# Performance work log

Hardware: AMD Instinct MI355X
Metric: run time of the kernel (lower is better)

The kernel has to match this reference:

```python
import jax, jax.numpy as jnp
import numpy as np
import math

B, S, D = 2, 2048, 1024
H, HKV = 16, 4
HD = D // H
NREP = H // HKV
E, TOPK, SHARED = 8, 2, 1
HIDDEN = 684
AUX_COEF = 0.01
RMS_EPS = 1e-5


def setup_inputs() -> dict:
    key = jax.random.key(0)
    ks = jax.random.split(key, 14)
    def w(k, shape):
        return jax.random.normal(k, shape, jnp.float32) * 0.02
    # standard RoPE angles, base 10000
    t = jnp.arange(S, dtype=jnp.float32)
    inv = 1.0 / (10000.0 ** (jnp.arange(0, HD, 2, dtype=jnp.float32) / HD))
    ang = t[:, None] * inv[None, :]  # [S, HD//2]
    return {
        "x": jax.random.normal(ks[0], (B, S, D), jnp.float32),
        "freqs_cos": jnp.cos(ang),
        "freqs_sin": jnp.sin(ang),
        "wq": w(ks[1], (D, D)),
        "wk": w(ks[2], (D, HKV * HD)),
        "wv": w(ks[3], (D, HKV * HD)),
        "wo": w(ks[4], (D, D)),
        "router_w": w(ks[5], (D, E)),
        "ew1": w(ks[6], (E, D, HIDDEN)),
        "ew2": w(ks[7], (E, HIDDEN, D)),
        "ew3": w(ks[8], (E, D, HIDDEN)),
        "sw1": w(ks[9], (SHARED, D, HIDDEN)),
        "sw2": w(ks[10], (SHARED, HIDDEN, D)),
        "sw3": w(ks[11], (SHARED, D, HIDDEN)),
        "g_attn": jnp.ones((D,), jnp.float32),
        "g_ffn": jnp.ones((D,), jnp.float32),
        "start_pos": 0,
    }


def rmsnorm(x, g, eps=RMS_EPS):
    xf = x.astype(jnp.float32)
    n = xf * jax.lax.rsqrt(jnp.mean(xf * xf, axis=-1, keepdims=True) + eps)
    return g * n.astype(x.dtype)


def rope(x, cos, sin):
    # pairs are consecutive elements (view_as_complex of reshape(..., -1, 2))
    xr, xi = x[..., 0::2], x[..., 1::2]
    c = cos[None, :, None, :]  # [1,S,1,HD//2]
    s = sin[None, :, None, :]
    r = xr * c - xi * s
    i = xr * s + xi * c
    return jnp.stack([r, i], axis=-1).reshape(x.shape)


def attention(x, freqs_cos, freqs_sin, wq, wk, wv, wo):
    b, s, d = x.shape
    q = (x @ wq).reshape(b, s, H, HD)
    k = (x @ wk).reshape(b, s, HKV, HD)
    v = (x @ wv).reshape(b, s, HKV, HD)
    q = rope(q, freqs_cos, freqs_sin)
    k = rope(k, freqs_cos, freqs_sin)
    k = jnp.repeat(k, NREP, axis=2)
    v = jnp.repeat(v, NREP, axis=2)
    q, k, v = (t.transpose(0, 2, 1, 3) for t in (q, k, v))  # [B,H,S,HD]
    att = jnp.einsum('bhqd,bhkd->bhqk', q, k) * (1.0 / math.sqrt(HD))
    # faithful to torch: tril then masked_fill(att == 0, -inf)
    tri = jnp.tril(jnp.ones((s, s), bool))
    att = jnp.where(tri, att, 0.0)
    att = jnp.where(att == 0.0, -jnp.inf, att)
    att = jax.nn.softmax(att, axis=-1)
    out = jnp.einsum('bhqk,bhkd->bhqd', att, v)
    out = out.transpose(0, 2, 1, 3).reshape(b, s, d)
    return out @ wo


def moe(x, router_w, ew1, ew2, ew3, sw1, sw2, sw3):
    b, s, d = x.shape
    xf = x.reshape(-1, d)                       # [N, D]
    logits = xf @ router_w                      # [N, E]
    probs = jax.nn.softmax(logits, axis=-1)
    _, topk_idx = jax.lax.top_k(logits, TOPK)   # [N, K]
    topk_p, _ = jax.lax.top_k(probs, TOPK)      # same ordering (softmax monotone)
    density = jnp.mean(jax.nn.one_hot(topk_idx[:, 0], E, dtype=jnp.float32), axis=0)
    aux = AUX_COEF * jnp.sum(density * jnp.mean(probs, axis=0)) * E
    # per-token combine weight over experts [N, E]
    onehot = jax.nn.one_hot(topk_idx, E, dtype=xf.dtype)  # [N, K, E]
    cw = jnp.einsum('nk,nke->ne', topk_p, onehot)
    # dense expert evaluation (jit-friendly dispatch/combine equivalent)
    h = jax.nn.silu(jnp.einsum('nd,edh->neh', xf, ew1)) * jnp.einsum('nd,edh->neh', xf, ew3)
    eo = jnp.einsum('neh,ehd->ned', h, ew2)
    out = jnp.einsum('ne,ned->nd', cw, eo)
    for i in range(SHARED):
        out = out + (jax.nn.silu(xf @ sw1[i]) * (xf @ sw3[i])) @ sw2[i]
    return out.reshape(b, s, d), aux


def reference(x, freqs_cos, freqs_sin, wq, wk, wv, wo, router_w, ew1, ew2, ew3, sw1, sw2, sw3, g_attn, g_ffn, start_pos):
    h = x + attention(rmsnorm(x, g_attn), freqs_cos, freqs_sin, wq, wk, wv, wo)
    ffn_out, aux = moe(rmsnorm(h, g_ffn), router_w, ew1, ew2, ew3, sw1, sw2, sw3)
    return h + ffn_out, aux
```

## Files before the change

### kernel.cpp

```cpp
#include <hip/hip_runtime.h>
#include <hip/hip_bf16.h>
#include <cstdint>

#define B_ 2
#define S_ 2048
#define D_ 1024
#define H_ 16
#define HKV_ 4
#define HD_ 64
#define E_ 8
#define HIDDEN_ 684
#define NT_ (B_*S_)
#define NEGBIG (-1e30f)

using bf16 = __hip_bfloat16;
typedef __attribute__((ext_vector_type(8))) short short8v;
typedef __attribute__((ext_vector_type(4))) short short4v;
typedef __attribute__((ext_vector_type(4))) float f32x4;

static __device__ __forceinline__ float b2f(bf16 v){ return __bfloat162float(v); }
static __device__ __forceinline__ bf16 f2b(float v){ return __float2bfloat16(v); }
static __device__ __forceinline__ short f2bs(float v){ bf16 h = f2b(v); return *reinterpret_cast<short*>(&h); }
static __device__ __forceinline__ float dload(const void* p, size_t i, int isbf){
  return isbf ? b2f(((const bf16*)p)[i]) : ((const float*)p)[i];
}

__global__ void k_detect(const uint32_t* __restrict__ g, int* __restrict__ flag, int* __restrict__ cnt){
  if(threadIdx.x == 0 && blockIdx.x == 0){
    uint32_t w0 = g[0], w1 = g[1], w2 = g[2], w3 = g[3];
    int bf;
    if(w0==0x3F803F80u && w1==0x3F803F80u && w2==0x3F803F80u && w3==0x3F803F80u) bf = 1;
    else if(w0==0x3F800000u && w1==0x3F800000u && w2==0x3F800000u && w3==0x3F800000u) bf = 0;
    else bf = 1;
    flag[0] = bf;
  }
  if(threadIdx.x < E_ && blockIdx.x == 0) cnt[threadIdx.x] = 0;
}

__global__ __launch_bounds__(256) void k_rms(const void* __restrict__ X, const void* __restrict__ g,
                                             bf16* __restrict__ outb, float* __restrict__ outf,
                                             const int* __restrict__ flag, int xdyn){
  int isbf = flag[0]; int xb = xdyn ? isbf : 0;
  int t = blockIdx.x; int tid = threadIdx.x;
  float v[4]; float ss = 0.f;
  #pragma unroll
  for(int i=0;i<4;i++){ v[i] = dload(X, (size_t)t*D_ + tid + i*256, xb); ss += v[i]*v[i]; }
  __shared__ float red[256];
  red[tid] = ss; __syncthreads();
  for(int st=128; st>0; st>>=1){ if(tid<st) red[tid] += red[tid+st]; __syncthreads(); }
  float r = rsqrtf(red[0]*(1.f/(float)D_) + 1e-5f);
  #pragma unroll
  for(int i=0;i<4;i++){
    int d = tid + i*256;
    float val = v[i]*r*dload(g, d, isbf);
    outb[(size_t)t*D_ + d] = f2b(val);
    if(outf) outf[(size_t)t*D_ + d] = val;
  }
}

#define ASTRIDE 40

static __device__ __forceinline__ f32x4 mfma16(short8v a, short8v b, f32x4 c){
  return __builtin_amdgcn_mfma_f32_16x16x32_bf16(a, b, c, 0, 0, 0);
}

template<int AMAP, int OMODE>
__global__ __launch_bounds__(256) void k_mgemm(
    const bf16* __restrict__ A, const void* __restrict__ Bw, void* __restrict__ Cout,
    const void* __restrict__ resid,
    int M, int N, int K, int ldc,
    const int* __restrict__ cnt, const int* __restrict__ offs, const int* __restrict__ list,
    const int* __restrict__ flag)
{
  int isbf = flag[0];
  int e, ct, rt;
  int base = 0; size_t eoff = 0;
  if(cnt){
    e = blockIdx.x;
    int nc = (N+63)>>6;
    ct = blockIdx.y % nc; rt = blockIdx.y / nc;
    M = cnt[e]; if(M<0) M=0; if(M>NT_) M=NT_;
    base = offs[e];
    eoff = (size_t)e*(size_t)K*(size_t)N;
  } else {
    e = 0; ct = blockIdx.x; rt = blockIdx.y;
  }
  int m0 = rt*128; if(m0 >= M) return;
  int n0 = ct*64;

  __shared__ short As[2][128*ASTRIDE];
  __shared__ short Bs[2][64*ASTRIDE];
  __shared__ int rowA[128];

  int tid = threadIdx.x;
  int w = tid>>6, l = tid&63, lr = l&15, lg = l>>4;

  if(tid < 128){
    int rloc = m0 + tid;
    int ar = -1;
    if(rloc < M) ar = (AMAP==2) ? (list[e*NT_ + rloc]>>1) : (base + rloc);
    rowA[tid] = ar;
  }
  __syncthreads();

  int srow = tid>>1, skh = (tid&1)*16;
  int keya = (srow>>4)&3, kb0 = skh>>3;
  int bk = tid>>3, bnc = (tid&7)*8;
  int keyb = ((tid&7)>>1)&3;
  int bcol = (((bk>>3)^keyb)<<3) + (bk&7);
  int arow = rowA[srow];

  short8v rA0, rA1, rB;

  auto loadAB = [&](int kt){
    int k0 = kt*32;
    {
      short tmp[16];
      if(arow >= 0 && k0+skh+16 <= K){
        const short4v* src = (const short4v*)(A + (size_t)arow*K + k0 + skh);
        #pragma unroll
        for(int c=0;c<4;c++) *(short4v*)&tmp[c*4] = src[c];
      } else {
        #pragma unroll
        for(int i=0;i<16;i++){
          int gk = k0+skh+i;
          short v = 0;
          if(arow>=0 && gk<K) v = *(const short*)&A[(size_t)arow*K+gk];
          tmp[i] = v;
        }
      }
      #pragma unroll
      for(int i=0;i<8;i++){ rA0[i]=tmp[i]; rA1[i]=tmp[8+i]; }
    }
    {
      int gk = k0 + bk;
      short tmp[8];
      if(gk < K && n0+bnc+8 <= N){
        size_t bb = eoff + (size_t)gk*N + n0 + bnc;
        if(isbf){
          const short4v* src = (const short4v*)((const bf16*)Bw + bb);
          *(short4v*)&tmp[0] = src[0];
          *(short4v*)&tmp[4] = src[1];
        } else {
          const f32x4* src = (const f32x4*)((const float*)Bw + bb);
          f32x4 f0 = src[0], f1 = src[1];
          #pragma unroll
          for(int i=0;i<4;i++){ tmp[i]=f2bs(f0[i]); tmp[4+i]=f2bs(f1[i]); }
        }
      } else {
        #pragma unroll
        for(int i=0;i<8;i++){
          int gn = n0+bnc+i;
          float v = 0.f;
          if(gk<K && gn<N) v = dload(Bw, eoff + (size_t)gk*N + gn, isbf);
          tmp[i] = f2bs(v);
        }
      }
      #pragma unroll
      for(int i=0;i<8;i++) rB[i]=tmp[i];
    }
  };
  auto writeAB = [&](int buf){
    *(short8v*)&As[buf][srow*ASTRIDE + ((kb0^keya)<<3)]     = rA0;
    *(short8v*)&As[buf][srow*ASTRIDE + (((kb0+1)^keya)<<3)] = rA1;
    #pragma unroll
    for(int i=0;i<8;i++) Bs[buf][(bnc+i)*ASTRIDE + bcol] = rB[i];
  };

  f32x4 acc[2][4] = {};
  int KT = (K+31)>>5;

  loadAB(0); writeAB(0);
  __syncthreads();
  int cur = 0;
  for(int kt=0; kt<KT; ++kt){
    bool more = (kt+1 < KT);
    if(more) loadAB(kt+1);
    short8v a[2], b[4];
    #pragma unroll
    for(int fi=0;fi<2;fi++)
      a[fi] = *(const short8v*)&As[cur][(w*32+fi*16+lr)*ASTRIDE + ((lg^((w*2+fi)&3))<<3)];
    #pragma unroll
    for(int fj=0;fj<4;fj++)
      b[fj] = *(const short8v*)&Bs[cur][(fj*16+lr)*ASTRIDE + ((lg^fj)<<3)];
    #pragma unroll
    for(int fi=0;fi<2;fi++)
      #pragma unroll
      for(int fj=0;fj<4;fj++)
        acc[fi][fj] = mfma16(a[fi], b[fj], acc[fi][fj]);
    if(more){ writeAB(cur^1); cur ^= 1; }
    __syncthreads();
  }

  #pragma unroll
  for(int fi=0;fi<2;fi++){
    #pragma unroll
    for(int r=0;r<4;r++){
      int rl = m0 + w*32 + fi*16 + lg*4 + r;
      if(rl >= M) continue;
      int orow;
      if(OMODE==2){ orow = list[e*NT_ + rl]; if(orow<0||orow>=2*NT_) continue; }
      else orow = base + rl;
      #pragma unroll
      for(int fj=0;fj<4;fj++){
        int gcol = n0 + fj*16 + lr;
        if(gcol >= N) continue;
        float v = acc[fi][fj][r];
        size_t o = (size_t)orow*ldc + gcol;
        if(OMODE==1)      ((float*)Cout)[o] = v + dload(resid, o, isbf);
        else if(OMODE==2) ((bf16*)Cout)[o] = f2b(v);
        else if(OMODE==3) ((float*)Cout)[o] = ((float*)Cout)[o] + v;
        else              ((bf16*)Cout)[o] = f2b(v);
      }
    }
  }
}

__global__ __launch_bounds__(256) void k_qkv(
    const bf16* __restrict__ A, const void* __restrict__ Wq, const void* __restrict__ Wk,
    const void* __restrict__ Wv, bf16* __restrict__ Oq, bf16* __restrict__ Ok, bf16* __restrict__ Ov,
    const int* __restrict__ flag)
{
  int isbf = flag[0];
  int ct = blockIdx.x, rt = blockIdx.y;
  const void* Bw; bf16* Cout; int N, n0;
  if(ct < 16){ Bw = Wq; Cout = Oq; N = D_;  n0 = ct*64; }
  else if(ct < 20){ Bw = Wk; Cout = Ok; N = 256; n0 = (ct-16)*64; }
  else { Bw = Wv; Cout = Ov; N = 256; n0 = (ct-20)*64; }
  const int K = D_, M = NT_;
  int m0 = rt*128;

  __shared__ short As[2][128*ASTRIDE];
  __shared__ short Bs[2][64*ASTRIDE];

  int tid = threadIdx.x;
  int w = tid>>6, l = tid&63, lr = l&15, lg = l>>4;

  int srow = tid>>1, skh = (tid&1)*16;
  int keya = (srow>>4)&3, kb0 = skh>>3;
  int bk = tid>>3, bnc = (tid&7)*8;
  int keyb = ((tid&7)>>1)&3;
  int bcol = (((bk>>3)^keyb)<<3) + (bk&7);
  int arow = m0 + srow;

  short8v rA0, rA1, rB;

  auto loadAB = [&](int kt){
    int k0 = kt*32;
    {
      short tmp[16];
      const short4v* src = (const short4v*)(A + (size_t)arow*K + k0 + skh);
      #pragma unroll
      for(int c=0;c<4;c++) *(short4v*)&tmp[c*4] = src[c];
      #pragma unroll
      for(int i=0;i<8;i++){ rA0[i]=tmp[i]; rA1[i]=tmp[8+i]; }
    }
    {
      int gk = k0 + bk;
      short tmp[8];
      size_t bb = (size_t)gk*N + n0 + bnc;
      if(isbf){
        const short4v* src = (const short4v*)((const bf16*)Bw + bb);
        *(short4v*)&tmp[0] = src[0];
        *(short4v*)&tmp[4] = src[1];
      } else {
        const f32x4* src = (const f32x4*)((const float*)Bw + bb);
        f32x4 f0 = src[0], f1 = src[1];
        #pragma unroll
        for(int i=0;i<4;i++){ tmp[i]=f2bs(f0[i]); tmp[4+i]=f2bs(f1[i]); }
      }
      #pragma unroll
      for(int i=0;i<8;i++) rB[i]=tmp[i];
    }
  };
  auto writeAB = [&](int buf){
    *(short8v*)&As[buf][srow*ASTRIDE + ((kb0^keya)<<3)]     = rA0;
    *(short8v*)&As[buf][srow*ASTRIDE + (((kb0+1)^keya)<<3)] = rA1;
    #pragma unroll
    for(int i=0;i<8;i++) Bs[buf][(bnc+i)*ASTRIDE + bcol] = rB[i];
  };

  f32x4 acc[2][4] = {};
  int KT = K>>5;

  loadAB(0); writeAB(0);
  __syncthreads();
  int cur = 0;
  for(int kt=0; kt<KT; ++kt){
    bool more = (kt+1 < KT);
    if(more) loadAB(kt+1);
    short8v a[2], b[4];
    #pragma unroll
    for(int fi=0;fi<2;fi++)
      a[fi] = *(const short8v*)&As[cur][(w*32+fi*16+lr)*ASTRIDE + ((lg^((w*2+fi)&3))<<3)];
    #pragma unroll
    for(int fj=0;fj<4;fj++)
      b[fj] = *(const short8v*)&Bs[cur][(fj*16+lr)*ASTRIDE + ((lg^fj)<<3)];
    #pragma unroll
    for(int fi=0;fi<2;fi++)
      #pragma unroll
      for(int fj=0;fj<4;fj++)
        acc[fi][fj] = mfma16(a[fi], b[fj], acc[fi][fj]);
    if(more){ writeAB(cur^1); cur ^= 1; }
    __syncthreads();
  }

  #pragma unroll
  for(int fi=0;fi<2;fi++){
    #pragma unroll
    for(int r=0;r<4;r++){
      int rl = m0 + w*32 + fi*16 + lg*4 + r;
      if(rl >= M) continue;
      #pragma unroll
      for(int fj=0;fj<4;fj++){
        int gcol = n0 + fj*16 + lr;
        Cout[(size_t)rl*N + gcol] = f2b(acc[fi][fj][r]);
      }
    }
  }
}

__global__ __launch_bounds__(256) void k_ffn1m(
    const bf16* __restrict__ A, const void* __restrict__ W1e, const void* __restrict__ W3e,
    const void* __restrict__ W1s, const void* __restrict__ W3s,
    bf16* __restrict__ OutE, bf16* __restrict__ OutS,
    const int* __restrict__ cnt, const int* __restrict__ offs, const int* __restrict__ list,
    const int* __restrict__ flag)
{
  int isbf = flag[0];
  const int K = D_, N = HIDDEN_;
  int e = blockIdx.x, y = blockIdx.y;
  int ct, rt, M, base, gat;
  const void* W1; const void* W3; bf16* Out;
  size_t eoff;
  if(y < 352){
    ct = y / 32; rt = y % 32;
    M = cnt[e]; if(M<0) M=0; if(M>NT_) M=NT_;
    base = offs[e]; gat = 1;
    W1 = W1e; W3 = W3e; Out = OutE;
    eoff = (size_t)e*(size_t)K*(size_t)N;
  } else {
    int ys = (y-352)*8 + e;
    ct = ys / 32; rt = ys % 32;
    M = NT_; base = 0; gat = 0;
    W1 = W1s; W3 = W3s; Out = OutS;
    eoff = 0;
  }
  int m0 = rt*128; if(m0 >= M) return;
  int n0 = ct*64;

  __shared__ short As[2][128*ASTRIDE];
  __shared__ short B1s[2][64*ASTRIDE];
  __shared__ short B3s[2][64*ASTRIDE];
  __shared__ int rowA[128];

  int tid = threadIdx.x;
  int w = tid>>6, l = tid&63, lr = l&15, lg = l>>4;

  if(tid < 128){
    int rloc = m0 + tid;
    int ar = -1;
    if(rloc < M) ar = gat ? (list[e*NT_ + rloc]>>1) : rloc;
    rowA[tid] = ar;
  }
  __syncthreads();

  int srow = tid>>1, skh = (tid&1)*16;
  int keya = (srow>>4)&3, kb0 = skh>>3;
  int bk = tid>>3, bnc = (tid&7)*8;
  int keyb = ((tid&7)>>1)&3;
  int bcol = (((bk>>3)^keyb)<<3) + (bk&7);
  int arow = rowA[srow];

  short8v rA0, rA1, rB1, rB3;

  auto loadB = [&](const void* Bw, int kt, short8v& rB){
    int k0 = kt*32;
    int gk = k0 + bk;
    short tmp[8];
    if(gk < K && n0+bnc+8 <= N){
      size_t bb = eoff + (size_t)gk*N + n0 + bnc;
      if(isbf){
        const short4v* src = (const short4v*)((const bf16*)Bw + bb);
        *(short4v*)&tmp[0] = src[0];
        *(short4v*)&tmp[4] = src[1];
      } else {
        const f32x4* src = (const f32x4*)((const float*)Bw + bb);
        f32x4 f0 = src[0], f1 = src[1];
        #pragma unroll
        for(int i=0;i<4;i++){ tmp[i]=f2bs(f0[i]); tmp[4+i]=f2bs(f1[i]); }
      }
    } else {
      #pragma unroll
      for(int i=0;i<8;i++){
        int gn = n0+bnc+i;
        float v = 0.f;
        if(gk<K && gn<N) v = dload(Bw, eoff + (size_t)gk*N + gn, isbf);
        tmp[i] = f2bs(v);
      }
    }
    #pragma unroll
    for(int i=0;i<8;i++) rB[i]=tmp[i];
  };
  auto loadA = [&](int kt){
    int k0 = kt*32;
    short tmp[16];
    if(arow >= 0 && k0+skh+16 <= K){
      const short4v* src = (const short4v*)(A + (size_t)arow*K + k0 + skh);
      #pragma unroll
      for(int c=0;c<4;c++) *(short4v*)&tmp[c*4] = src[c];
    } else {
      #pragma unroll
      for(int i=0;i<16;i++){
        int gk = k0+skh+i;
        short v = 0;
        if(arow>=0 && gk<K) v = *(const short*)&A[(size_t)arow*K+gk];
        tmp[i] = v;
      }
    }
    #pragma unroll
    for(int i=0;i<8;i++){ rA0[i]=tmp[i]; rA1[i]=tmp[8+i]; }
  };
  auto writeAll = [&](int buf){
    *(short8v*)&As[buf][srow*ASTRIDE + ((kb0^keya)<<3)]     = rA0;
    *(short8v*)&As[buf][srow*ASTRIDE + (((kb0+1)^keya)<<3)] = rA1;
    #pragma unroll
    for(int i=0;i<8;i++){
      B1s[buf][(bnc+i)*ASTRIDE + bcol] = rB1[i];
      B3s[buf][(bnc+i)*ASTRIDE + bcol] = rB3[i];
    }
  };

  f32x4 a1[2][4] = {}, a3[2][4] = {};
  int KT = (K+31)>>5;

  loadA(0); loadB(W1, 0, rB1); loadB(W3, 0, rB3); writeAll(0);
  __syncthreads();
  int cur = 0;
  for(int kt=0; kt<KT; ++kt){
    bool more = (kt+1 < KT);
    if(more){ loadA(kt+1); loadB(W1, kt+1, rB1); loadB(W3, kt+1, rB3); }
    short8v a[2], b1[4], b3[4];
    #pragma unroll
    for(int fi=0;fi<2;fi++)
      a[fi] = *(const short8v*)&As[cur][(w*32+fi*16+lr)*ASTRIDE + ((lg^((w*2+fi)&3))<<3)];
    #pragma unroll
    for(int fj=0;fj<4;fj++){
      b1[fj] = *(const short8v*)&B1s[cur][(fj*16+lr)*ASTRIDE + ((lg^fj)<<3)];
      b3[fj] = *(const short8v*)&B3s[cur][(fj*16+lr)*ASTRIDE + ((lg^fj)<<3)];
    }
    #pragma unroll
    for(int fi=0;fi<2;fi++)
      #pragma unroll
      for(int fj=0;fj<4;fj++){
        a1[fi][fj] = mfma16(a[fi], b1[fj], a1[fi][fj]);
        a3[fi][fj] = mfma16(a[fi], b3[fj], a3[fi][fj]);
      }
    if(more){ writeAll(cur^1); cur ^= 1; }
    __syncthreads();
  }

  #pragma unroll
  for(int fi=0;fi<2;fi++){
    #pragma unroll
    for(int r=0;r<4;r++){
      int rl = m0 + w*32 + fi*16 + lg*4 + r;
      if(rl >= M) continue;
      int orow = base + rl;
      #pragma unroll
      for(int fj=0;fj<4;fj++){
        int gcol = n0 + fj*16 + lr;
        if(gcol >= N) continue;
        float sg = a1[fi][fj][r];
        float v = (sg/(1.f+__expf(-sg))) * a3[fi][fj][r];
        Out[(size_t)orow*N + gcol] = f2b(v);
      }
    }
  }
}

__global__ __launch_bounds__(256) void k_ffn2m(
    const bf16* __restrict__ Ae, const bf16* __restrict__ Ash,
    const void* __restrict__ W2e, const void* __restrict__ W2s,
    bf16* __restrict__ OutE, float* __restrict__ OutS,
    const int* __restrict__ cnt, const int* __restrict__ offs, const int* __restrict__ list,
    const int* __restrict__ flag)
{
  int isbf = flag[0];
  const int K = HIDDEN_, N = D_;
  int e = blockIdx.x, y = blockIdx.y;
  int ct, rt, M, base, exm;
  const bf16* A; const void* Bw;
  size_t eoff;
  if(y < 512){
    ct = y / 32; rt = y % 32;
    M = cnt[e]; if(M<0) M=0; if(M>NT_) M=NT_;
    base = offs[e]; exm = 1;
    A = Ae; Bw = W2e;
    eoff = (size_t)e*(size_t)K*(size_t)N;
  } else {
    int ys = (y-512)*8 + e;
    ct = ys / 32; rt = ys % 32;
    M = NT_; base = 0; exm = 0;
    A = Ash; Bw = W2s;
    eoff = 0;
  }
  int m0 = rt*128; if(m0 >= M) return;
  int n0 = ct*64;

  __shared__ short As[2][128*ASTRIDE];
  __shared__ short Bs[2][64*ASTRIDE];

  int tid = threadIdx.x;
  int w = tid>>6, l = tid&63, lr = l&15, lg = l>>4;

  int srow = tid>>1, skh = (tid&1)*16;
  int keya = (srow>>4)&3, kb0 = skh>>3;
  int bk = tid>>3, bnc = (tid&7)*8;
  int keyb = ((tid&7)>>1)&3;
  int bcol = (((bk>>3)^keyb)<<3) + (bk&7);
  int arow = (m0 + srow < M) ? (base + m0 + srow) : -1;

  short8v rA0, rA1, rB;

  auto loadAB = [&](int kt){
    int k0 = kt*32;
    {
      short tmp[16];
      if(arow >= 0 && k0+skh+16 <= K){
        const short4v* src = (const short4v*)(A + (size_t)arow*K + k0 + skh);
        #pragma unroll
        for(int c=0;c<4;c++) *(short4v*)&tmp[c*4] = src[c];
      } else {
        #pragma unroll
        for(int i=0;i<16;i++){
          int gk = k0+skh+i;
          short v = 0;
          if(arow>=0 && gk<K) v = *(const short*)&A[(size_t)arow*K+gk];
          tmp[i] = v;
        }
      }
      #pragma unroll
      for(int i=0;i<8;i++){ rA0[i]=tmp[i]; rA1[i]=tmp[8+i]; }
    }
    {
      int gk = k0 + bk;
      short tmp[8];
      if(gk < K && n0+bnc+8 <= N){
        size_t bb = eoff + (size_t)gk*N + n0 + bnc;
        if(isbf){
          const short4v* src = (const short4v*)((const bf16*)Bw + bb);
          *(short4v*)&tmp[0] = src[0];
          *(short4v*)&tmp[4] = src[1];
        } else {
          const f32x4* src = (const f32x4*)((const float*)Bw + bb);
          f32x4 f0 = src[0], f1 = src[1];
          #pragma unroll
          for(int i=0;i<4;i++){ tmp[i]=f2bs(f0[i]); tmp[4+i]=f2bs(f1[i]); }
        }
      } else {
        #pragma unroll
        for(int i=0;i<8;i++){
          int gn = n0+bnc+i;
          float v = 0.f;
          if(gk<K && gn<N) v = dload(Bw, eoff + (size_t)gk*N + gn, isbf);
          tmp[i] = f2bs(v);
        }
      }
      #pragma unroll
      for(int i=0;i<8;i++) rB[i]=tmp[i];
    }
  };
  auto writeAB = [&](int buf){
    *(short8v*)&As[buf][srow*ASTRIDE + ((kb0^keya)<<3)]     = rA0;
    *(short8v*)&As[buf][srow*ASTRIDE + (((kb0+1)^keya)<<3)] = rA1;
    #pragma unroll
    for(int i=0;i<8;i++) Bs[buf][(bnc+i)*ASTRIDE + bcol] = rB[i];
  };

  f32x4 acc[2][4] = {};
  int KT = (K+31)>>5;

  loadAB(0); writeAB(0);
  __syncthreads();
  int cur = 0;
  for(int kt=0; kt<KT; ++kt){
    bool more = (kt+1 < KT);
    if(more) loadAB(kt+1);
    short8v a[2], b[4];
    #pragma unroll
    for(int fi=0;fi<2;fi++)
      a[fi] = *(const short8v*)&As[cur][(w*32+fi*16+lr)*ASTRIDE + ((lg^((w*2+fi)&3))<<3)];
    #pragma unroll
    for(int fj=0;fj<4;fj++)
      b[fj] = *(const short8v*)&Bs[cur][(fj*16+lr)*ASTRIDE + ((lg^fj)<<3)];
    #pragma unroll
    for(int fi=0;fi<2;fi++)
      #pragma unroll
      for(int fj=0;fj<4;fj++)
        acc[fi][fj] = mfma16(a[fi], b[fj], acc[fi][fj]);
    if(more){ writeAB(cur^1); cur ^= 1; }
    __syncthreads();
  }

  #pragma unroll
  for(int fi=0;fi<2;fi++){
    #pragma unroll
    for(int r=0;r<4;r++){
      int rl = m0 + w*32 + fi*16 + lg*4 + r;
      if(rl >= M) continue;
      if(exm){
        int orow = list[e*NT_ + rl];
        if(orow<0||orow>=2*NT_) continue;
        #pragma unroll
        for(int fj=0;fj<4;fj++){
          int gcol = n0 + fj*16 + lr;
          OutE[(size_t)orow*N + gcol] = f2b(acc[fi][fj][r]);
        }
      } else {
        #pragma unroll
        for(int fj=0;fj<4;fj++){
          int gcol = n0 + fj*16 + lr;
          size_t o = (size_t)rl*N + gcol;
          OutS[o] = OutS[o] + acc[fi][fj][r];
        }
      }
    }
  }
}

__global__ __launch_bounds__(256) void k_rope(bf16* __restrict__ ql, bf16* __restrict__ kl,
                                              const void* __restrict__ fc, const void* __restrict__ fs,
                                              const int* __restrict__ flag){
  int isbf = flag[0];
  int t = blockIdx.x; int s = t % S_;
  int tid = threadIdx.x;
  for(int p0 = tid; p0 < 512; p0 += 256){
    int h = p0>>5, p = p0&31;
    float c = dload(fc, s*32+p, isbf), sn = dload(fs, s*32+p, isbf);
    size_t o = (size_t)t*D_ + h*64 + 2*p;
    float xr = b2f(ql[o]), xi = b2f(ql[o+1]);
    ql[o]   = f2b(xr*c - xi*sn);
    ql[o+1] = f2b(xr*sn + xi*c);
  }
  if(tid < 128){
    int h = tid>>5, p = tid&31;
    float c = dload(fc, s*32+p, isbf), sn = dload(fs, s*32+p, isbf);
    size_t o = (size_t)t*256 + h*64 + 2*p;
    float xr = b2f(kl[o]), xi = b2f(kl[o+1]);
    kl[o]   = f2b(xr*c - xi*sn);
    kl[o+1] = f2b(xr*sn + xi*c);
  }
}

#define TST 72

__global__ __launch_bounds__(256) void k_attn(const bf16* __restrict__ Q, const bf16* __restrict__ Kg,
                                              const bf16* __restrict__ V, bf16* __restrict__ Out){
  int qt_ = (S_/64 - 1) - blockIdx.x;
  int h = blockIdx.y, b = blockIdx.z;
  int kvh = h>>2;
  const bf16* qb = Q + (size_t)b*S_*D_ + h*HD_;
  const bf16* kb = Kg + (size_t)b*S_*256 + kvh*HD_;
  const bf16* vb = V  + (size_t)b*S_*256 + kvh*HD_;
  __shared__ short Qs[64*TST];
  __shared__ short Ks[64*TST];
  __shared__ short Vt[64*TST];
  __shared__ short Ps[4][16*TST];
  int tid = threadIdx.x;
  int w = tid>>6, l = tid&63, lr = l&15, lg = l>>4;
  int sr = tid>>2, sc0 = (tid&3)*16;
  int vc = (((sr>>3)^(tid&3))<<3) + (sr&7);

  {
    const short8v* src = (const short8v*)(qb + (size_t)(qt_*64 + sr)*D_ + sc0);
    *(short8v*)&Qs[sr*TST + sc0]     = src[0];
    *(short8v*)&Qs[sr*TST + sc0 + 8] = src[1];
  }
  __syncthreads();
  short8v aQ0 = *(const short8v*)&Qs[(w*16+lr)*TST + lg*8];
  short8v aQ1 = *(const short8v*)&Qs[(w*16+lr)*TST + lg*8 + 32];

  float mreg[4], lreg[4];
  f32x4 accO[4] = {};
  #pragma unroll
  for(int r=0;r<4;r++){ mreg[r] = NEGBIG; lreg[r] = 0.f; }

  for(int kt=0; kt<=qt_; ++kt){
    __syncthreads();
    {
      const short8v* ksrc = (const short8v*)(kb + (size_t)(kt*64 + sr)*256 + sc0);
      *(short8v*)&Ks[sr*TST + sc0]     = ksrc[0];
      *(short8v*)&Ks[sr*TST + sc0 + 8] = ksrc[1];
      const short8v* vsrc = (const short8v*)(vb + (size_t)(kt*64 + sr)*256 + sc0);
      short8v v0 = vsrc[0], v1 = vsrc[1];
      #pragma unroll
      for(int i=0;i<8;i++){
        Vt[(sc0+i)*TST + vc]   = v0[i];
        Vt[(sc0+8+i)*TST + vc] = v1[i];
      }
    }
    __syncthreads();
    f32x4 s[4];
    #pragma unroll
    for(int fj=0; fj<4; fj++){
      short8v b0 = *(const short8v*)&Ks[(fj*16+lr)*TST + lg*8];
      short8v b1 = *(const short8v*)&Ks[(fj*16+lr)*TST + lg*8 + 32];
      f32x4 z = {};
      z = mfma16(aQ0, b0, z);
      z = mfma16(aQ1, b1, z);
      s[fj] = z;
    }
    #pragma unroll
    for(int fj=0; fj<4; fj++)
      #pragma unroll
      for(int r=0;r<4;r++){
        float v = s[fj][r]*0.125f;
        if(kt==qt_ && (fj*16+lr) > (w*16+lg*4+r)) v = NEGBIG;
        s[fj][r] = v;
      }
    float p[4][4], sc[4];
    #pragma unroll
    for(int r=0;r<4;r++){
      float mx = fmaxf(fmaxf(s[0][r],s[1][r]), fmaxf(s[2][r],s[3][r]));
      mx = fmaxf(mx, __shfl_xor(mx,1,64));
      mx = fmaxf(mx, __shfl_xor(mx,2,64));
      mx = fmaxf(mx, __shfl_xor(mx,4,64));
      mx = fmaxf(mx, __shfl_xor(mx,8,64));
      float mn = fmaxf(mreg[r], mx);
      sc[r] = __expf(mreg[r]-mn);
      float ps = 0.f;
      #pragma unroll
      for(int fj=0;fj<4;fj++){ float pv = __expf(s[fj][r]-mn); p[fj][r] = pv; ps += pv; }
      ps += __shfl_xor(ps,1,64); ps += __shfl_xor(ps,2,64);
      ps += __shfl_xor(ps,4,64); ps += __shfl_xor(ps,8,64);
      lreg[r] = lreg[r]*sc[r] + ps;
      mreg[r] = mn;
    }
    #pragma unroll
    for(int fj=0;fj<4;fj++)
      #pragma unroll
      for(int r=0;r<4;r++)
        accO[fj][r] *= sc[r];
    #pragma unroll
    for(int fj=0;fj<4;fj++)
      #pragma unroll
      for(int r=0;r<4;r++)
        Ps[w][(lg*4+r)*TST + fj*16+lr] = f2bs(p[fj][r]);
    short8v a0 = *(const short8v*)&Ps[w][lr*TST + lg*8];
    short8v a1 = *(const short8v*)&Ps[w][lr*TST + lg*8 + 32];
    #pragma unroll
    for(int fj=0;fj<4;fj++){
      int row = fj*16+lr;
      short8v b0 = *(const short8v*)&Vt[row*TST + ((lg^fj)<<3)];
      short8v b1 = *(const short8v*)&Vt[row*TST + (((lg^fj)+4)<<3)];
      accO[fj] = mfma16(a0, b0, accO[fj]);
      accO[fj] = mfma16(a1, b1, accO[fj]);
    }
  }
  #pragma unroll
  for(int r=0;r<4;r++){
    int qr = qt_*64 + w*16 + lg*4 + r;
    float inv = (lreg[r] > 0.f) ? 1.f/lreg[r] : 0.f;
    #pragma unroll
    for(int fj=0;fj<4;fj++)
      Out[((size_t)(b*S_+qr))*D_ + h*HD_ + fj*16+lr] = f2b(accO[fj][r]*inv);
  }
}

__global__ __launch_bounds__(64) void k_router(const float* __restrict__ X, const void* __restrict__ W,
                                               float* __restrict__ probs, float* __restrict__ p01,
                                               int* __restrict__ idx0buf, int* __restrict__ list,
                                               int* __restrict__ cnt, const int* __restrict__ flag){
  int isbf = flag[0];
  int t = blockIdx.x; int lane = threadIdx.x;
  float pe[8] = {};
  if(isbf){
    const bf16* Wb = (const bf16*)W;
    for(int d = lane; d < D_; d += 64){
      float xv = X[(size_t)t*D_ + d];
      #pragma unroll
      for(int e=0;e<8;e++) pe[e] += xv*b2f(Wb[(size_t)d*E_+e]);
    }
  } else {
    const float* Wf = (const float*)W;
    for(int d = lane; d < D_; d += 64){
      float xv = X[(size_t)t*D_ + d];
      #pragma unroll
      for(int e=0;e<8;e++) pe[e] += xv*Wf[(size_t)d*E_+e];
    }
  }
  for(int msk=1;msk<64;msk<<=1)
    #pragma unroll
    for(int e=0;e<8;e++) pe[e] += __shfl_xor(pe[e], msk, 64);
  if(lane == 0){
    float mx = pe[0];
    #pragma unroll
    for(int e=1;e<8;e++) mx = fmaxf(mx, pe[e]);
    float pr[8], sum = 0.f;
    #pragma unroll
    for(int e=0;e<8;e++){ pr[e] = __expf(pe[e]-mx); sum += pr[e]; }
    #pragma unroll
    for(int e=0;e<8;e++){ pr[e] /= sum; probs[t*8+e] = pr[e]; }
    int i0 = 0;
    #pragma unroll
    for(int e=1;e<8;e++) if(pe[e] > pe[i0]) i0 = e;
    int i1 = -1;
    #pragma unroll
    for(int e=0;e<8;e++){ if(e==i0) continue; if(i1<0 || pe[e] > pe[i1]) i1 = e; }
    p01[t*2]   = pr[i0];
    p01[t*2+1] = pr[i1];
    idx0buf[t] = i0;
    int pos = atomicAdd(&cnt[i0], 1);
    if(pos >= 0 && pos < NT_) list[i0*NT_ + pos] = t*2;
    pos     = atomicAdd(&cnt[i1], 1);
    if(pos >= 0 && pos < NT_) list[i1*NT_ + pos] = t*2 + 1;
  }
}

__global__ __launch_bounds__(256) void k_stats(const float* __restrict__ probs, const int* __restrict__ idx0buf,
                                               float* __restrict__ cnt0f, float* __restrict__ psum){
  int e = blockIdx.x; int tid = threadIdx.x;
  float sp = 0.f, sc = 0.f;
  for(int n = tid; n < NT_; n += 256){ sp += probs[n*8+e]; sc += (idx0buf[n]==e) ? 1.f : 0.f; }
  __shared__ float r1[256], r2[256];
  r1[tid] = sp; r2[tid] = sc; __syncthreads();
  for(int st=128; st>0; st>>=1){ if(tid<st){ r1[tid]+=r1[tid+st]; r2[tid]+=r2[tid+st]; } __syncthreads(); }
  if(tid==0){ psum[e] = r1[0]; cnt0f[e] = r2[0]; }
}

__global__ void k_finish(const float* __restrict__ cnt0f, const float* __restrict__ psum,
                         const int* __restrict__ cnt, int* __restrict__ offs,
                         bf16* __restrict__ auxb, float* __restrict__ auxf, const int* __restrict__ flag){
  if(threadIdx.x==0 && blockIdx.x==0){
    int o = 0;
    for(int e=0;e<8;e++){ offs[e] = o; int c = cnt[e]; if(c < 0) c = 0; if(c > NT_) c = NT_; o += c; }
    float aux = 0.f;
    for(int e=0;e<8;e++) aux += (cnt0f[e]*(1.f/(float)NT_))*(psum[e]*(1.f/(float)NT_));
    float v = aux*0.01f*8.f;
    if(flag[0]) auxb[0] = f2b(v); else auxf[0] = v;
  }
}

__global__ __launch_bounds__(256) void k_combine(const float* __restrict__ hbuf, const bf16* __restrict__ eosl,
                                                 const float* __restrict__ p01,
                                                 bf16* __restrict__ outb, float* __restrict__ outf,
                                                 const int* __restrict__ flag){
  int t = blockIdx.x; int tid = threadIdx.x;
  int isbf = flag[0];
  float p0 = p01[t*2], p1 = p01[t*2+1];
  #pragma unroll
  for(int i=0;i<4;i++){
    int d = tid + i*256;
    float v = hbuf[(size_t)t*D_ + d]
            + p0*b2f(eosl[((size_t)(t*2))*D_ + d])
            + p1*b2f(eosl[((size_t)(t*2+1))*D_ + d]);
    size_t o = (size_t)t*D_ + d;
    if(isbf) outb[o] = f2b(v); else outf[o] = v;
  }
}

static const size_t O_HBUF = 0;
static const size_t O_XNB  = 16777216;
static const size_t O_QLIN = 25165824;
static const size_t O_KLIN = 33554432;
static const size_t O_VLIN = 35651584;
static const size_t O_AOUT = 37748736;
static const size_t O_XN2B = 16777216;
static const size_t O_XN2F = 25165824;
static const size_t O_HEXP = 46137344;
static const size_t O_SHH  = 57344000;
static const size_t O_EOSL = 16777216;
static const size_t O_PROBS= 62947328;
static const size_t O_P01  = 63078400;
static const size_t O_IDX0 = 63111168;
static const size_t O_LIST = 63127552;
static const size_t O_CNT  = 63258624;
static const size_t O_CNT0 = 63258656;
static const size_t O_PSUM = 63258688;
static const size_t O_OFFS = 63258720;
static const size_t O_FLAG = 63258752;

extern "C" void kernel_launch(void* const* d_in, const int* in_sizes, int n_in,
                              void* d_out, int out_size, void* d_ws, size_t ws_size,
                              hipStream_t stream){
  (void)in_sizes; (void)n_in; (void)out_size; (void)ws_size;
  char* ws = (char*)d_ws;
  float* hbuf = (float*)(ws + O_HBUF);
  bf16* xnb   = (bf16*)(ws + O_XNB);
  bf16* qlin  = (bf16*)(ws + O_QLIN);
  bf16* klin  = (bf16*)(ws + O_KLIN);
  bf16* vlin  = (bf16*)(ws + O_VLIN);
  bf16* aout  = (bf16*)(ws + O_AOUT);
  bf16* xn2b  = (bf16*)(ws + O_XN2B);
  float* xn2f = (float*)(ws + O_XN2F);
  bf16* hexp  = (bf16*)(ws + O_HEXP);
  bf16* shh   = (bf16*)(ws + O_SHH);
  bf16* eosl  = (bf16*)(ws + O_EOSL);
  float* probs=(float*)(ws + O_PROBS);
  float* p01 = (float*)(ws + O_P01);
  int*  idx0 = (int*)(ws + O_IDX0);
  int*  list = (int*)(ws + O_LIST);
  int*  cnt  = (int*)(ws + O_CNT);
  float* cnt0f=(float*)(ws + O_CNT0);
  float* psum= (float*)(ws + O_PSUM);
  int*  offs = (int*)(ws + O_OFFS);
  int*  flg  = (int*)(ws + O_FLAG);

  bf16* outb = (bf16*)d_out;
  float* outf = (float*)d_out;
  bf16* auxb = outb + (size_t)NT_*D_;
  float* auxf = outf + (size_t)NT_*D_;

  k_detect<<<1, 64, 0, stream>>>((const uint32_t*)d_in[14], flg, cnt);

  k_rms<<<NT_, 256, 0, stream>>>(d_in[0], d_in[14], xnb, nullptr, flg, 1);

  k_qkv<<<dim3(24,32), 256, 0, stream>>>(xnb, d_in[3], d_in[4], d_in[5], qlin, klin, vlin, flg);

  k_rope<<<NT_, 256, 0, stream>>>(qlin, klin, d_in[1], d_in[2], flg);

  k_attn<<<dim3(S_/64, H_, B_), 256, 0, stream>>>(qlin, klin, vlin, aout);

  k_mgemm<0,1><<<dim3(16,32), 256, 0, stream>>>(aout, d_in[6], hbuf, d_in[0], NT_, D_, D_, D_, nullptr, nullptr, nullptr, flg);

  k_rms<<<NT_, 256, 0, stream>>>(hbuf, d_in[15], xn2b, xn2f, flg, 0);

  k_router<<<NT_, 64, 0, stream>>>(xn2f, d_in[7], probs, p01, idx0, list, cnt, flg);
  k_stats<<<E_, 256, 0, stream>>>(probs, idx0, cnt0f, psum);
  k_finish<<<1, 64, 0, stream>>>(cnt0f, psum, cnt, offs, auxb, auxf, flg);

  k_ffn1m<<<dim3(E_, 352+44), 256, 0, stream>>>(xn2b, d_in[8], d_in[10], d_in[11], d_in[13],
                                                hexp, shh, cnt, offs, list, flg);

  k_ffn2m<<<dim3(E_, 512+64), 256, 0, stream>>>(hexp, shh, d_in[9], d_in[12],
                                                eosl, hbuf, cnt, offs, list, flg);

  k_combine<<<NT_, 256, 0, stream>>>(hbuf, eosl, p01, outb, outf, flg);
}
```

Measured before the change: 625.0 us.

## Unroll FFN GEMM K-loops by two with dual register prefetch sets

Both FFN GEMM kernels (gate/up and down projection) now unroll the K loop by two and keep two register staging sets. Global loads for tile kt+2 and kt+3 are issued while the MFMAs on the current shared-memory buffer run, so shared-memory writes and global reads are spread further ahead of their use. The aim is to hide global-load latency better and drop the per-iteration buffer-index toggling. In exchange it adds register pressure, which could lower occupancy. It also assumes an even tile count, which holds for K=1024 and K=684.

```diff
diff --git a/kernel.cpp b/kernel.cpp
--- a/kernel.cpp
+++ b/kernel.cpp
@@ -372,8 +372,6 @@
   int bcol = (((bk>>3)^keyb)<<3) + (bk&7);
   int arow = rowA[srow];
 
-  short8v rA0, rA1, rB1, rB3;
-
   auto loadB = [&](const void* Bw, int kt, short8v& rB){
     int k0 = kt*32;
     int gk = k0 + bk;
@@ -402,7 +400,7 @@
     #pragma unroll
     for(int i=0;i<8;i++) rB[i]=tmp[i];
   };
-  auto loadA = [&](int kt){
+  auto loadA = [&](int kt, short8v& x0, short8v& x1){
     int k0 = kt*32;
     short tmp[16];
     if(arow >= 0 && k0+skh+16 <= K){
@@ -419,44 +417,58 @@
       }
     }
     #pragma unroll
-    for(int i=0;i<8;i++){ rA0[i]=tmp[i]; rA1[i]=tmp[8+i]; }
-  };
-  auto writeAll = [&](int buf){
-    *(short8v*)&As[buf][srow*ASTRIDE + ((kb0^keya)<<3)]     = rA0;
-    *(short8v*)&As[buf][srow*ASTRIDE + (((kb0+1)^keya)<<3)] = rA1;
+    for(int i=0;i<8;i++){ x0[i]=tmp[i]; x1[i]=tmp[8+i]; }
+  };
+  auto writeSet = [&](int buf, short8v& a0, short8v& a1, short8v& b1, short8v& b3){
+    *(short8v*)&As[buf][srow*ASTRIDE + ((kb0^keya)<<3)]     = a0;
+    *(short8v*)&As[buf][srow*ASTRIDE + (((kb0+1)^keya)<<3)] = a1;
     #pragma unroll
     for(int i=0;i<8;i++){
-      B1s[buf][(bnc+i)*ASTRIDE + bcol] = rB1[i];
-      B3s[buf][(bnc+i)*ASTRIDE + bcol] = rB3[i];
-    }
-  };
-
-  f32x4 a1[2][4] = {}, a3[2][4] = {};
+      B1s[buf][(bnc+i)*ASTRIDE + bcol] = b1[i];
+      B3s[buf][(bnc+i)*ASTRIDE + bcol] = b3[i];
+    }
+  };
+
+  f32x4 a1c[2][4] = {}, a3c[2][4] = {};
   int KT = (K+31)>>5;
 
-  loadA(0); loadB(W1, 0, rB1); loadB(W3, 0, rB3); writeAll(0);
+  short8v xA0, xA1, xB1, xB3;
+  short8v yA0, yA1, yB1, yB3;
+
+  auto mfmaStep = [&](int buf){
+    short8v a[2], b1f[4], b3f[4];
+    #pragma unroll
+    for(int fi=0;fi<2;fi++)
+      a[fi] = *(const short8v*)&As[buf][(w*32+fi*16+lr)*ASTRIDE + ((lg^((w*2+fi)&3))<<3)];
+    #pragma unroll
+    for(int fj=0;fj<4;fj++){
+      b1f[fj] = *(const short8v*)&B1s[buf][(fj*16+lr)*ASTRIDE + ((lg^fj)<<3)];
+      b3f[fj] = *(const short8v*)&B3s[buf][(fj*16+lr)*ASTRIDE + ((lg^fj)<<3)];
+    }
+    #pragma unroll
+    for(int fi=0;fi<2;fi++)
+      #pragma unroll
+      for(int fj=0;fj<4;fj++){
+        a1c[fi][fj] = mfma16(a[fi], b1f[fj], a1c[fi][fj]);
+        a3c[fi][fj] = mfma16(a[fi], b3f[fj], a3c[fi][fj]);
+      }
+  };
+
+  loadA(0, xA0, xA1); loadB(W1, 0, xB1); loadB(W3, 0, xB3);
+  writeSet(0, xA0, xA1, xB1, xB3);
+  loadA(1, yA0, yA1); loadB(W1, 1, yB1); loadB(W3, 1, yB3);
   __syncthreads();
-  int cur = 0;
-  for(int kt=0; kt<KT; ++kt){
-    bool more = (kt+1 < KT);
-    if(more){ loadA(kt+1); loadB(W1, kt+1, rB1); loadB(W3, kt+1, rB3); }
-    short8v a[2], b1[4], b3[4];
-    #pragma unroll
-    for(int fi=0;fi<2;fi++)
-      a[fi] = *(const short8v*)&As[cur][(w*32+fi*16+lr)*ASTRIDE + ((lg^((w*2+fi)&3))<<3)];
-    #pragma unroll
-    for(int fj=0;fj<4;fj++){
-      b1[fj] = *(const short8v*)&B1s[cur][(fj*16+lr)*ASTRIDE + ((lg^fj)<<3)];
-      b3[fj] = *(const short8v*)&B3s[cur][(fj*16+lr)*ASTRIDE + ((lg^fj)<<3)];
-    }
-    #pragma unroll
-    for(int fi=0;fi<2;fi++)
-      #pragma unroll
-      for(int fj=0;fj<4;fj++){
-        a1[fi][fj] = mfma16(a[fi], b1[fj], a1[fi][fj]);
-        a3[fi][fj] = mfma16(a[fi], b3[fj], a3[fi][fj]);
-      }
-    if(more){ writeAll(cur^1); cur ^= 1; }
+
+  for(int kt=0; kt<KT; kt+=2){
+    mfmaStep(0);
+    writeSet(1, yA0, yA1, yB1, yB3);
+    if(kt+2 < KT){ loadA(kt+2, xA0, xA1); loadB(W1, kt+2, xB1); loadB(W3, kt+2, xB3); }
+    __syncthreads();
+    mfmaStep(1);
+    if(kt+2 < KT){
+      writeSet(0, xA0, xA1, xB1, xB3);
+      if(kt+3 < KT){ loadA(kt+3, yA0, yA1); loadB(W1, kt+3, yB1); loadB(W3, kt+3, yB3); }
+    }
     __syncthreads();
   }
 
@@ -471,8 +483,8 @@
       for(int fj=0;fj<4;fj++){
         int gcol = n0 + fj*16 + lr;
         if(gcol >= N) continue;
-        float sg = a1[fi][fj][r];
-        float v = (sg/(1.f+__expf(-sg))) * a3[fi][fj][r];
+        float sg = a1c[fi][fj][r];
+        float v = (sg/(1.f+__expf(-sg))) * a3c[fi][fj][r];
         Out[(size_t)orow*N + gcol] = f2b(v);
       }
     }
@@ -521,85 +533,96 @@
   int bcol = (((bk>>3)^keyb)<<3) + (bk&7);
   int arow = (m0 + srow < M) ? (base + m0 + srow) : -1;
 
-  short8v rA0, rA1, rB;
-
-  auto loadAB = [&](int kt){
+  auto loadA = [&](int kt, short8v& x0, short8v& x1){
     int k0 = kt*32;
-    {
-      short tmp[16];
-      if(arow >= 0 && k0+skh+16 <= K){
-        const short4v* src = (const short4v*)(A + (size_t)arow*K + k0 + skh);
+    short tmp[16];
+    if(arow >= 0 && k0+skh+16 <= K){
+      const short4v* src = (const short4v*)(A + (size_t)arow*K + k0 + skh);
+      #pragma unroll
+      for(int c=0;c<4;c++) *(short4v*)&tmp[c*4] = src[c];
+    } else {
+      #pragma unroll
+      for(int i=0;i<16;i++){
+        int gk = k0+skh+i;
+        short v = 0;
+        if(arow>=0 && gk<K) v = *(const short*)&A[(size_t)arow*K+gk];
+        tmp[i] = v;
+      }
+    }
+    #pragma unroll
+    for(int i=0;i<8;i++){ x0[i]=tmp[i]; x1[i]=tmp[8+i]; }
+  };
+  auto loadB = [&](int kt, short8v& rB){
+    int k0 = kt*32;
+    int gk = k0 + bk;
+    short tmp[8];
+    if(gk < K && n0+bnc+8 <= N){
+      size_t bb = eoff + (size_t)gk*N + n0 + bnc;
+      if(isbf){
+        const short4v* src = (const short4v*)((const bf16*)Bw + bb);
+        *(short4v*)&tmp[0] = src[0];
+        *(short4v*)&tmp[4] = src[1];
+      } else {
+        const f32x4* src = (const f32x4*)((const float*)Bw + bb);
+        f32x4 f0 = src[0], f1 = src[1];
         #pragma unroll
-        for(int c=0;c<4;c++) *(short4v*)&tmp[c*4] = src[c];
-      } else {
-        #pragma unroll
-        for(int i=0;i<16;i++){
-          int gk = k0+skh+i;
-          short v = 0;
-          if(arow>=0 && gk<K) v = *(const short*)&A[(size_t)arow*K+gk];
-          tmp[i] = v;
-        }
-      }
-      #pragma unroll
-      for(int i=0;i<8;i++){ rA0[i]=tmp[i]; rA1[i]=tmp[8+i]; }
-    }
-    {
-      int gk = k0 + bk;
-      short tmp[8];
-      if(gk < K && n0+bnc+8 <= N){
-        size_t bb = eoff + (size_t)gk*N + n0 + bnc;
-        if(isbf){
-          const short4v* src = (const short4v*)((const bf16*)Bw + bb);
-          *(short4v*)&tmp[0] = src[0];
-          *(short4v*)&tmp[4] = src[1];
-        } else {
-          const f32x4* src = (const f32x4*)((const float*)Bw + bb);
-          f32x4 f0 = src[0], f1 = src[1];
-          #pragma unroll
-          for(int i=0;i<4;i++){ tmp[i]=f2bs(f0[i]); tmp[4+i]=f2bs(f1[i]); }
-        }
-      } else {
-        #pragma unroll
-        for(int i=0;i<8;i++){
-          int gn = n0+bnc+i;
-          float v = 0.f;
-          if(gk<K && gn<N) v = dload(Bw, eoff + (size_t)gk*N + gn, isbf);
-          tmp[i] = f2bs(v);
-        }
-      }
-      #pragma unroll
-      for(int i=0;i<8;i++) rB[i]=tmp[i];
-    }
-  };
-  auto writeAB = [&](int buf){
-    *(short8v*)&As[buf][srow*ASTRIDE + ((kb0^keya)<<3)]     = rA0;
-    *(short8v*)&As[buf][srow*ASTRIDE + (((kb0+1)^keya)<<3)] = rA1;
-    #pragma unroll
-    for(int i=0;i<8;i++) Bs[buf][(bnc+i)*ASTRIDE + bcol] = rB[i];
+        for(int i=0;i<4;i++){ tmp[i]=f2bs(f0[i]); tmp[4+i]=f2bs(f1[i]); }
+      }
+    } else {
+      #pragma unroll
+      for(int i=0;i<8;i++){
+        int gn = n0+bnc+i;
+        float v = 0.f;
+        if(gk<K && gn<N) v = dload(Bw, eoff + (size_t)gk*N + gn, isbf);
+        tmp[i] = f2bs(v);
+      }
+    }
+    #pragma unroll
+    for(int i=0;i<8;i++) rB[i]=tmp[i];
+  };
+  auto writeSet = [&](int buf, short8v& a0, short8v& a1, short8v& b){
+    *(short8v*)&As[buf][srow*ASTRIDE + ((kb0^keya)<<3)]     = a0;
+    *(short8v*)&As[buf][srow*ASTRIDE + (((kb0+1)^keya)<<3)] = a1;
+    #pragma unroll
+    for(int i=0;i<8;i++) Bs[buf][(bnc+i)*ASTRIDE + bcol] = b[i];
   };
 
   f32x4 acc[2][4] = {};
   int KT = (K+31)>>5;
 
-  loadAB(0); writeAB(0);
-  __syncthreads();
-  int cur = 0;
-  for(int kt=0; kt<KT; ++kt){
-    bool more = (kt+1 < KT);
-    if(more) loadAB(kt+1);
+  short8v xA0, xA1, xB;
+  short8v yA0, yA1, yB;
+
+  auto mfmaStep = [&](int buf){
     short8v a[2], b[4];
     #pragma unroll
     for(int fi=0;fi<2;fi++)
-      a[fi] = *(const short8v*)&As[cur][(w*32+fi*16+lr)*ASTRIDE + ((lg^((w*2+fi)&3))<<3)];
+      a[fi] = *(const short8v*)&As[buf][(w*32+fi*16+lr)*ASTRIDE + ((lg^((w*2+fi)&3))<<3)];
     #pragma unroll
     for(int fj=0;fj<4;fj++)
-      b[fj] = *(const short8v*)&Bs[cur][(fj*16+lr)*ASTRIDE + ((lg^fj)<<3)];
+      b[fj] = *(const short8v*)&Bs[buf][(fj*16+lr)*ASTRIDE + ((lg^fj)<<3)];
     #pragma unroll
     for(int fi=0;fi<2;fi++)
       #pragma unroll
       for(int fj=0;fj<4;fj++)
         acc[fi][fj] = mfma16(a[fi], b[fj], acc[fi][fj]);
-    if(more){ writeAB(cur^1); cur ^= 1; }
+  };
+
+  loadA(0, xA0, xA1); loadB(0, xB);
+  writeSet(0, xA0, xA1, xB);
+  loadA(1, yA0, yA1); loadB(1, yB);
+  __syncthreads();
+
+  for(int kt=0; kt<KT; kt+=2){
+    mfmaStep(0);
+    writeSet(1, yA0, yA1, yB);
+    if(kt+2 < KT){ loadA(kt+2, xA0, xA1); loadB(kt+2, xB); }
+    __syncthreads();
+    mfmaStep(1);
+    if(kt+2 < KT){
+      writeSet(0, xA0, xA1, xB);
+      if(kt+3 < KT){ loadA(kt+3, yA0, yA1); loadB(kt+3, yB); }
+    }
     __syncthreads();
   }
 
```

New measurement: 657.1 us. +5.1%, slower.
